# Performance work log

Hardware: AMD Instinct MI355X
Metric: run time of the kernel (lower is better)

## Reference

```python
import jax, jax.numpy as jnp
import numpy as np

EPS = 1e-7  # keras backend epsilon


def _tril_indices(stack_size: int) -> np.ndarray:
    # matches np.nonzero(np.tri(S, S, -1).ravel())[0] in build()
    return np.nonzero(np.tri(stack_size, stack_size, -1).ravel())[0]


def setup_inputs() -> dict:
    key = jax.random.key(0)
    x = jax.random.normal(key, (8, 512, 256), dtype=jnp.float32)
    return {"x": x}


def reference(x) -> jnp.ndarray:
    B, S, D = x.shape
    tril = jnp.asarray(_tril_indices(S))  # static, length S*(S-1)/2
    # pairwise squared L2 over feature dim: (B, S, S, D) -> (B, S, S)
    diff = x[:, :, None, :] - x[:, None, :, :]
    d2 = jnp.sum(jnp.square(diff), axis=-1)
    d = jnp.sqrt(jnp.maximum(d2, EPS))
    # flatten the S x S matrix and gather strict lower-triangular entries
    out = d.reshape(B, S * S)[:, tril]  # (B, S*(S-1)/2)
    return out
```

## Files before the change

kernel.cpp:

```cpp
#include <hip/hip_runtime.h>
#include <math.h>

#define BB 8
#define SS 512
#define DD 256
#define PP (SS * (SS - 1) / 2)
#define STRIPS 16
#define SUPER_PER_B (STRIPS * (STRIPS + 1) / 2)

typedef short bf16x8 __attribute__((ext_vector_type(8)));
typedef float f32x4 __attribute__((ext_vector_type(4)));

static __device__ inline unsigned short f2bf(float f) {
    unsigned int u = __float_as_uint(f);
    unsigned int r = u + 0x7fffu + ((u >> 16) & 1u);
    return (unsigned short)(r >> 16);
}

__global__ __launch_bounds__(256) void prep_kernel(const float* __restrict__ x,
                                                   unsigned short* __restrict__ xb,
                                                   float* __restrict__ norms) {
    int row  = blockIdx.x * 4 + (threadIdx.x >> 6);
    int lane = threadIdx.x & 63;
    const float4* src = reinterpret_cast<const float4*>(x + (size_t)row * DD) + lane;
    float4 v = *src;
    float ss = v.x * v.x + v.y * v.y + v.z * v.z + v.w * v.w;
    ushort4 pk;
    pk.x = f2bf(v.x); pk.y = f2bf(v.y); pk.z = f2bf(v.z); pk.w = f2bf(v.w);
    *reinterpret_cast<ushort4*>(xb + (size_t)row * DD + lane * 4) = pk;
    #pragma unroll
    for (int o = 32; o > 0; o >>= 1) ss += __shfl_down(ss, o);
    if (lane == 0) norms[row] = ss;
}

__global__ __launch_bounds__(256) void dist_kernel(const unsigned short* __restrict__ xb,
                                                   const float* __restrict__ norms,
                                                   float* __restrict__ out) {
    int w    = blockIdx.x * 4 + (threadIdx.x >> 6);
    int lane = threadIdx.x & 63;
    int b    = w / SUPER_PER_B;
    int s    = w - b * SUPER_PER_B;
    int ti = (int)((sqrtf(8.0f * (float)s + 1.0f) - 1.0f) * 0.5f);
    while ((ti + 1) * (ti + 2) / 2 <= s) ti++;
    while (ti * (ti + 1) / 2 > s) ti--;
    int tj = s - ti * (ti + 1) / 2;

    int r16 = lane & 15;
    int kq  = lane >> 4;

    const unsigned short* base = xb + (size_t)b * SS * DD;
    const unsigned short* a0r = base + (size_t)(ti * 32 + r16) * DD + kq * 8;
    const unsigned short* a1r = a0r + 16 * DD;
    const unsigned short* b0r = base + (size_t)(tj * 32 + r16) * DD + kq * 8;
    const unsigned short* b1r = b0r + 16 * DD;

    f32x4 acc00 = {0.f,0.f,0.f,0.f}, acc01 = {0.f,0.f,0.f,0.f};
    f32x4 acc10 = {0.f,0.f,0.f,0.f}, acc11 = {0.f,0.f,0.f,0.f};

    bf16x8 a0 = *reinterpret_cast<const bf16x8*>(a0r);
    bf16x8 a1 = *reinterpret_cast<const bf16x8*>(a1r);
    bf16x8 b0 = *reinterpret_cast<const bf16x8*>(b0r);
    bf16x8 b1 = *reinterpret_cast<const bf16x8*>(b1r);

    #pragma unroll
    for (int k = 32; k <= DD; k += 32) {
        bf16x8 na0, na1, nb0, nb1;
        if (k < DD) {
            na0 = *reinterpret_cast<const bf16x8*>(a0r + k);
            na1 = *reinterpret_cast<const bf16x8*>(a1r + k);
            nb0 = *reinterpret_cast<const bf16x8*>(b0r + k);
            nb1 = *reinterpret_cast<const bf16x8*>(b1r + k);
        }
        acc00 = __builtin_amdgcn_mfma_f32_16x16x32_bf16(a0, b0, acc00, 0, 0, 0);
        acc01 = __builtin_amdgcn_mfma_f32_16x16x32_bf16(a0, b1, acc01, 0, 0, 0);
        acc10 = __builtin_amdgcn_mfma_f32_16x16x32_bf16(a1, b0, acc10, 0, 0, 0);
        acc11 = __builtin_amdgcn_mfma_f32_16x16x32_bf16(a1, b1, acc11, 0, 0, 0);
        if (k < DD) { a0 = na0; a1 = na1; b0 = nb0; b1 = nb1; }
    }

    const float* nrm = norms + b * SS;
    float* outb = out + (size_t)b * PP;
    #pragma unroll
    for (int q = 0; q < 2; q++) {
        int jg = tj * 32 + q * 16 + r16;
        float nj = nrm[jg];
        const f32x4& accq0 = (q == 0) ? acc00 : acc01;
        const f32x4& accq1 = (q == 0) ? acc10 : acc11;
        #pragma unroll
        for (int p = 0; p < 2; p++) {
            const f32x4& a = (p == 0) ? accq0 : accq1;
            #pragma unroll
            for (int r = 0; r < 4; r++) {
                int ig = ti * 32 + p * 16 + kq * 4 + r;
                if (ig > jg) {
                    float ni = nrm[ig];
                    float d2 = ni + nj - 2.0f * a[r];
                    d2 = fmaxf(d2, 1e-7f);
                    outb[(size_t)(ig * (ig - 1) / 2) + jg] = sqrtf(d2);
                }
            }
        }
    }
}

extern "C" void kernel_launch(void* const* d_in, const int* in_sizes, int n_in,
                              void* d_out, int out_size, void* d_ws, size_t ws_size,
                              hipStream_t stream) {
    const float* x = (const float*)d_in[0];
    float* out = (float*)d_out;
    unsigned short* xb = (unsigned short*)d_ws;
    float* norms = (float*)((char*)d_ws + (size_t)BB * SS * DD * 2);

    prep_kernel<<<1024, 256, 0, stream>>>(x, xb, norms);
    dist_kernel<<<272, 256, 0, stream>>>(xb, norms, out);
}
```

Before: 69.11 us.

## Fuse bf16 conversion into distance kernel with 64-row LDS panels

Removes the separate prep kernel and its workspace round trip. Each block now loads 64-row fp32 panels of x, converts them to bf16 and computes row norms, then stages them in swizzled shared memory. Four waves split a 64x64 output tile and read their MFMA operands from LDS instead of global memory. The cost is that each block converts its panels again (each strip is staged by several blocks), and the grid is only 288 blocks using 64KB of LDS each.

New measurement: 73.57 us. +6.5%, slower.

```diff
diff --git a/kernel.cpp b/kernel.cpp
--- a/kernel.cpp
+++ b/kernel.cpp
@@ -5,8 +5,10 @@
 #define SS 512
 #define DD 256
 #define PP (SS * (SS - 1) / 2)
-#define STRIPS 16
-#define SUPER_PER_B (STRIPS * (STRIPS + 1) / 2)
+#define STRIP 64
+#define NSTRIP (SS / STRIP)
+#define SUPER_PER_B (NSTRIP * (NSTRIP + 1) / 2)
+#define NBLOCKS (BB * SUPER_PER_B)
 
 typedef short bf16x8 __attribute__((ext_vector_type(8)));
 typedef float f32x4 __attribute__((ext_vector_type(4)));
@@ -17,83 +19,99 @@
     return (unsigned short)(r >> 16);
 }
 
-__global__ __launch_bounds__(256) void prep_kernel(const float* __restrict__ x,
-                                                   unsigned short* __restrict__ xb,
-                                                   float* __restrict__ norms) {
-    int row  = blockIdx.x * 4 + (threadIdx.x >> 6);
-    int lane = threadIdx.x & 63;
-    const float4* src = reinterpret_cast<const float4*>(x + (size_t)row * DD) + lane;
-    float4 v = *src;
-    float ss = v.x * v.x + v.y * v.y + v.z * v.z + v.w * v.w;
-    ushort4 pk;
-    pk.x = f2bf(v.x); pk.y = f2bf(v.y); pk.z = f2bf(v.z); pk.w = f2bf(v.w);
-    *reinterpret_cast<ushort4*>(xb + (size_t)row * DD + lane * 4) = pk;
+static __device__ inline void stage_panel(const float* __restrict__ src,
+                                          unsigned short* panel, float* nrm,
+                                          int t, int lane) {
     #pragma unroll
-    for (int o = 32; o > 0; o >>= 1) ss += __shfl_down(ss, o);
-    if (lane == 0) norms[row] = ss;
+    for (int it = 0; it < 16; ++it) {
+        int f = it * 256 + t;
+        int r = f >> 6;
+        int q = f & 63;
+        float4 v = reinterpret_cast<const float4*>(src)[f];
+        float ss = v.x * v.x + v.y * v.y + v.z * v.z + v.w * v.w;
+        ushort4 pk;
+        pk.x = f2bf(v.x); pk.y = f2bf(v.y); pk.z = f2bf(v.z); pk.w = f2bf(v.w);
+        int c = q >> 1, h = q & 1;
+        int off = r * 512 + (((c ^ (r & 7)) << 4) | (h << 3));
+        *reinterpret_cast<ushort4*>(reinterpret_cast<char*>(panel) + off) = pk;
+        #pragma unroll
+        for (int o = 32; o > 0; o >>= 1) ss += __shfl_xor(ss, o);
+        if (lane == 0) nrm[r] = ss;
+    }
 }
 
-__global__ __launch_bounds__(256) void dist_kernel(const unsigned short* __restrict__ xb,
-                                                   const float* __restrict__ norms,
-                                                   float* __restrict__ out) {
-    int w    = blockIdx.x * 4 + (threadIdx.x >> 6);
-    int lane = threadIdx.x & 63;
-    int b    = w / SUPER_PER_B;
-    int s    = w - b * SUPER_PER_B;
+__global__ __launch_bounds__(256) void dist_fused(const float* __restrict__ x,
+                                                  float* __restrict__ out) {
+    __shared__ unsigned short pa[STRIP * DD];
+    __shared__ unsigned short pb[STRIP * DD];
+    __shared__ float na[STRIP];
+    __shared__ float nb[STRIP];
+
+    int t    = threadIdx.x;
+    int lane = t & 63;
+    int w    = t >> 6;
+
+    int bid = blockIdx.x;
+    int b   = bid / SUPER_PER_B;
+    int s   = bid - b * SUPER_PER_B;
     int ti = (int)((sqrtf(8.0f * (float)s + 1.0f) - 1.0f) * 0.5f);
     while ((ti + 1) * (ti + 2) / 2 <= s) ti++;
     while (ti * (ti + 1) / 2 > s) ti--;
     int tj = s - ti * (ti + 1) / 2;
 
+    const float* xa = x + (size_t)(b * SS + ti * STRIP) * DD;
+    stage_panel(xa, pa, na, t, lane);
+    if (ti != tj) {
+        const float* xbp = x + (size_t)(b * SS + tj * STRIP) * DD;
+        stage_panel(xbp, pb, nb, t, lane);
+    }
+    __syncthreads();
+
+    const unsigned short* PB = (ti == tj) ? pa : pb;
+    const float* NB          = (ti == tj) ? na : nb;
+
+    int wr  = w >> 1, wc = w & 1;
     int r16 = lane & 15;
     int kq  = lane >> 4;
+    int la0 = wr * 32 + r16, la1 = la0 + 16;
+    int lb0 = wc * 32 + r16, lb1 = lb0 + 16;
 
-    const unsigned short* base = xb + (size_t)b * SS * DD;
-    const unsigned short* a0r = base + (size_t)(ti * 32 + r16) * DD + kq * 8;
-    const unsigned short* a1r = a0r + 16 * DD;
-    const unsigned short* b0r = base + (size_t)(tj * 32 + r16) * DD + kq * 8;
-    const unsigned short* b1r = b0r + 16 * DD;
+    const char* cpa = reinterpret_cast<const char*>(pa);
+    const char* cpb = reinterpret_cast<const char*>(PB);
 
     f32x4 acc00 = {0.f,0.f,0.f,0.f}, acc01 = {0.f,0.f,0.f,0.f};
     f32x4 acc10 = {0.f,0.f,0.f,0.f}, acc11 = {0.f,0.f,0.f,0.f};
 
-    bf16x8 a0 = *reinterpret_cast<const bf16x8*>(a0r);
-    bf16x8 a1 = *reinterpret_cast<const bf16x8*>(a1r);
-    bf16x8 b0 = *reinterpret_cast<const bf16x8*>(b0r);
-    bf16x8 b1 = *reinterpret_cast<const bf16x8*>(b1r);
-
     #pragma unroll
-    for (int k = 32; k <= DD; k += 32) {
-        bf16x8 na0, na1, nb0, nb1;
-        if (k < DD) {
-            na0 = *reinterpret_cast<const bf16x8*>(a0r + k);
-            na1 = *reinterpret_cast<const bf16x8*>(a1r + k);
-            nb0 = *reinterpret_cast<const bf16x8*>(b0r + k);
-            nb1 = *reinterpret_cast<const bf16x8*>(b1r + k);
-        }
+    for (int stp = 0; stp < 8; ++stp) {
+        int c0 = kq + 4 * stp;
+        bf16x8 a0 = *reinterpret_cast<const bf16x8*>(cpa + la0 * 512 + ((c0 ^ (la0 & 7)) << 4));
+        bf16x8 a1 = *reinterpret_cast<const bf16x8*>(cpa + la1 * 512 + ((c0 ^ (la1 & 7)) << 4));
+        bf16x8 b0 = *reinterpret_cast<const bf16x8*>(cpb + lb0 * 512 + ((c0 ^ (lb0 & 7)) << 4));
+        bf16x8 b1 = *reinterpret_cast<const bf16x8*>(cpb + lb1 * 512 + ((c0 ^ (lb1 & 7)) << 4));
         acc00 = __builtin_amdgcn_mfma_f32_16x16x32_bf16(a0, b0, acc00, 0, 0, 0);
         acc01 = __builtin_amdgcn_mfma_f32_16x16x32_bf16(a0, b1, acc01, 0, 0, 0);
         acc10 = __builtin_amdgcn_mfma_f32_16x16x32_bf16(a1, b0, acc10, 0, 0, 0);
         acc11 = __builtin_amdgcn_mfma_f32_16x16x32_bf16(a1, b1, acc11, 0, 0, 0);
-        if (k < DD) { a0 = na0; a1 = na1; b0 = nb0; b1 = nb1; }
     }
 
-    const float* nrm = norms + b * SS;
     float* outb = out + (size_t)b * PP;
     #pragma unroll
-    for (int q = 0; q < 2; q++) {
-        int jg = tj * 32 + q * 16 + r16;
-        float nj = nrm[jg];
-        const f32x4& accq0 = (q == 0) ? acc00 : acc01;
-        const f32x4& accq1 = (q == 0) ? acc10 : acc11;
+    for (int q = 0; q < 2; ++q) {
+        int jgl = wc * 32 + q * 16 + r16;
+        int jg  = tj * STRIP + jgl;
+        float nj = NB[jgl];
         #pragma unroll
-        for (int p = 0; p < 2; p++) {
-            const f32x4& a = (p == 0) ? accq0 : accq1;
+        for (int p = 0; p < 2; ++p) {
+            f32x4 a;
+            if (q == 0) a = (p == 0) ? acc00 : acc10;
+            else        a = (p == 0) ? acc01 : acc11;
             #pragma unroll
-            for (int r = 0; r < 4; r++) {
-                int ig = ti * 32 + p * 16 + kq * 4 + r;
+            for (int r = 0; r < 4; ++r) {
+                int igl = wr * 32 + p * 16 + kq * 4 + r;
+                int ig  = ti * STRIP + igl;
                 if (ig > jg) {
-                    float ni = nrm[ig];
+                    float ni = na[igl];
                     float d2 = ni + nj - 2.0f * a[r];
                     d2 = fmaxf(d2, 1e-7f);
                     outb[(size_t)(ig * (ig - 1) / 2) + jg] = sqrtf(d2);
@@ -108,9 +126,6 @@
                               hipStream_t stream) {
     const float* x = (const float*)d_in[0];
     float* out = (float*)d_out;
-    unsigned short* xb = (unsigned short*)d_ws;
-    float* norms = (float*)((char*)d_ws + (size_t)BB * SS * DD * 2);
-
-    prep_kernel<<<1024, 256, 0, stream>>>(x, xb, norms);
-    dist_kernel<<<272, 256, 0, stream>>>(xb, norms, out);
+    (void)d_ws; (void)ws_size;
+    dist_fused<<<NBLOCKS, 256, 0, stream>>>(x, out);
 }
```
